# Kernel optimization log

Measured on AMD Instinct MI355X. Metric: run time of the kernel, lower is better.

Reference implementation:

```python
import jax, jax.numpy as jnp
import numpy as np

B, S, D, NL, H, KV, F, V, R = 4, 1024, 2048, 2, 16, 4, 8192, 32000, 16
HD = D // H                      # 128, Llama-3 head dim
LORA_SCALE = 32.0 / 16.0         # alpha / r
ROPE_THETA = 500000.0
EPS = 1e-5


def _rope_tables(seq_len, hd):
    inv = 1.0 / (ROPE_THETA ** (jnp.arange(0, hd, 2, dtype=jnp.float32) / hd))
    freqs = jnp.arange(seq_len, dtype=jnp.float32)[:, None] * inv[None, :]   # [S, hd/2]
    emb = jnp.concatenate([freqs, freqs], axis=-1)                           # [S, hd]
    return jnp.cos(emb), jnp.sin(emb)


def _apply_rope(x, cos, sin):
    # x: [B, S, nh, HD]; LLaMA rotate_half convention
    h = x.shape[-1] // 2
    rot = jnp.concatenate([-x[..., h:], x[..., :h]], axis=-1)
    return x * cos[None, :, None, :] + rot * sin[None, :, None, :]


def _rmsnorm(x, w):
    return x * jax.lax.rsqrt(jnp.mean(x * x, axis=-1, keepdims=True) + EPS) * w


def _forward(embed, wq, wk, wv, wo, laq, lbq, lav, lbv, wg, wu, wd, n1, n2, nf,
             input_ids, attention_mask):
    b, s = input_ids.shape
    cos, sin = _rope_tables(s, HD)
    amask = attention_mask.astype(bool)
    # causal AND key-padding mask: [B, 1, S, S]
    mask = jnp.tril(jnp.ones((s, s), bool))[None, None] & amask[:, None, None, :]
    x = embed[input_ids]                                   # [B, S, D]
    for l in range(NL):
        h = _rmsnorm(x, n1[l])
        # base projection + LoRA adapter (q and v only, as in target_modules)
        q = h @ wq[l] + ((h @ laq[l].T) @ lbq[l].T) * LORA_SCALE
        k = h @ wk[l]
        v = h @ wv[l] + ((h @ lav[l].T) @ lbv[l].T) * LORA_SCALE
        q = _apply_rope(q.reshape(b, s, H, HD), cos, sin)
        k = _apply_rope(k.reshape(b, s, KV, HD), cos, sin)
        v = v.reshape(b, s, KV, HD)
        k = jnp.repeat(k, H // KV, axis=2)                 # GQA expand
        v = jnp.repeat(v, H // KV, axis=2)
        scores = jnp.einsum('bqhd,bkhd->bhqk', q, k) / jnp.float32(np.sqrt(HD))
        scores = jnp.where(mask, scores, jnp.float32(-1e9))
        attn = jax.nn.softmax(scores, axis=-1)
        o = jnp.einsum('bhqk,bkhd->bqhd', attn, v).reshape(b, s, D)
        x = x + o @ wo[l]
        h2 = _rmsnorm(x, n2[l])
        x = x + (jax.nn.silu(h2 @ wg[l]) * (h2 @ wu[l])) @ wd[l]
    h = _rmsnorm(x, nf)                                    # final norm -> last_hidden_state
    m = attention_mask.astype(jnp.float32)[..., None]
    return (h * m).sum(axis=1) / jnp.clip(m.sum(axis=1), 1e-9)   # masked mean pool [B, D]


def setup_inputs() -> dict:
    key = jax.random.key(0)
    ks = jax.random.split(key, 14)
    sd = 0.02
    nrm = lambda k, shape: sd * jax.random.normal(k, shape, dtype=jnp.float32)
    return {
        'embed': nrm(ks[0], (V, D)),
        'wq': nrm(ks[1], (NL, D, D)),
        'wk': nrm(ks[2], (NL, D, KV * HD)),
        'wv': nrm(ks[3], (NL, D, KV * HD)),
        'wo': nrm(ks[4], (NL, D, D)),
        'laq': nrm(ks[5], (NL, R, D)),
        'lbq': nrm(ks[6], (NL, D, R)),
        'lav': nrm(ks[7], (NL, R, D)),
        'lbv': nrm(ks[8], (NL, KV * HD, R)),
        'wg': nrm(ks[9], (NL, D, F)),
        'wu': nrm(ks[10], (NL, D, F)),
        'wd': nrm(ks[11], (NL, F, D)),
        'n1': jnp.ones((NL, D), jnp.float32),
        'n2': jnp.ones((NL, D), jnp.float32),
        'nf': jnp.ones((D,), jnp.float32),
        'input_ids': jax.random.randint(ks[12], (B, S), 0, V, dtype=jnp.int32),
        'attention_mask': jnp.ones((B, S), jnp.int32),
    }


def reference(embed, wq, wk, wv, wo, laq, lbq, lav, lbv, wg, wu, wd, n1, n2, nf,
              input_ids, attention_mask):
    return _forward(embed, wq, wk, wv, wo, laq, lbq, lav, lbv, wg, wu, wd,
                    n1, n2, nf, input_ids, attention_mask)
```

## Files before the change

kernel.cpp:

```cpp
#include <hip/hip_runtime.h>
#include <math.h>

#define B_  4
#define S_  1024
#define D_  2048
#define NL_ 2
#define H_  16
#define KV_ 4
#define F_  8192
#define R_  16
#define HD_ 128
#define BS_ (B_*S_)
#define QT2 32
#define KBLK 64
#define NQKV 3072

typedef unsigned short u16;
typedef __attribute__((ext_vector_type(8))) __bf16 bf16x8;
typedef __attribute__((ext_vector_type(4))) float  f32x4;

__device__ __forceinline__ u16 f2bf(float f) {
    unsigned x = __float_as_uint(f);
    unsigned r = (x + 0x7fffu + ((x >> 16) & 1u)) >> 16;
    return (u16)r;
}
__device__ __forceinline__ float bf2f(u16 u) {
    return __uint_as_float(((unsigned)u) << 16);
}

__device__ __forceinline__ void gload16(const void* g, void* l) {
    __builtin_amdgcn_global_load_lds((const __attribute__((address_space(1))) void*)g,
                                     (__attribute__((address_space(3))) void*)l, 16, 0, 0);
}

__global__ void embed_kernel(const float* __restrict__ embed,
                             const int* __restrict__ ids,
                             float* __restrict__ x) {
    int tok = blockIdx.x;
    int id  = ids[tok];
    const float4* src = (const float4*)(embed + (size_t)id * D_);
    float4*       dst = (float4*)(x + (size_t)tok * D_);
    for (int i = threadIdx.x; i < D_/4; i += blockDim.x) dst[i] = src[i];
}

template<int OUTBF>
__global__ __launch_bounds__(256) void rmsnorm_kernel(const float* __restrict__ x,
                                                      const float* __restrict__ w,
                                                      void* __restrict__ out) {
    int row = blockIdx.x;
    const float4* xr = (const float4*)(x + (size_t)row * D_);
    float ss = 0.f;
    for (int i = threadIdx.x; i < D_/4; i += 256) {
        float4 v = xr[i];
        ss += v.x*v.x + v.y*v.y + v.z*v.z + v.w*v.w;
    }
    __shared__ float red[4];
    for (int off = 32; off; off >>= 1) ss += __shfl_down(ss, off);
    if ((threadIdx.x & 63) == 0) red[threadIdx.x >> 6] = ss;
    __syncthreads();
    float tot = red[0] + red[1] + red[2] + red[3];
    float scale = rsqrtf(tot / (float)D_ + 1e-5f);
    const float4* w4 = (const float4*)w;
    for (int i = threadIdx.x; i < D_/4; i += 256) {
        float4 v = xr[i], g = w4[i];
        float a = v.x*scale*g.x, b = v.y*scale*g.y, c = v.z*scale*g.z, d = v.w*scale*g.w;
        if (OUTBF) {
            ushort4 o; o.x = f2bf(a); o.y = f2bf(b); o.z = f2bf(c); o.w = f2bf(d);
            ((ushort4*)((u16*)out + (size_t)row * D_))[i] = o;
        } else {
            float4 o; o.x = a; o.y = b; o.z = c; o.w = d;
            ((float4*)((float*)out + (size_t)row * D_))[i] = o;
        }
    }
}

__global__ __launch_bounds__(256) void convt_kernel(const float* __restrict__ in,
                                                    u16* __restrict__ outT,
                                                    int K, int N) {
    __shared__ float tile[64][65];
    int k0 = blockIdx.y * 64, n0 = blockIdx.x * 64;
    int t = threadIdx.x, r = t >> 4, c4 = (t & 15) * 4;
    #pragma unroll
    for (int p = 0; p < 4; p++) {
        float4 v = *(const float4*)(in + (size_t)(k0 + p * 16 + r) * N + n0 + c4);
        tile[p*16+r][c4]   = v.x; tile[p*16+r][c4+1] = v.y;
        tile[p*16+r][c4+2] = v.z; tile[p*16+r][c4+3] = v.w;
    }
    __syncthreads();
    #pragma unroll
    for (int p = 0; p < 4; p++) {
        int n = p * 16 + r;
        ushort4 o;
        o.x = f2bf(tile[c4][n]);   o.y = f2bf(tile[c4+1][n]);
        o.z = f2bf(tile[c4+2][n]); o.w = f2bf(tile[c4+3][n]);
        *(ushort4*)(outT + (size_t)(n0 + n) * K + k0 + c4) = o;
    }
}

__global__ __launch_bounds__(256) void convt_qkv(const float* __restrict__ wq,
                                                 const float* __restrict__ wk,
                                                 const float* __restrict__ wv,
                                                 const float* __restrict__ wo,
                                                 u16* __restrict__ outT) {
    int z = blockIdx.z;
    int N = (z == 0 || z == 3) ? 2048 : 512;
    if (blockIdx.x * 64 >= N) return;
    const float* in = (z == 0) ? wq : (z == 1 ? wk : (z == 2 ? wv : wo));
    size_t roff = (z == 0) ? 0 : (z == 1 ? 2048 : (z == 2 ? 2560 : 3072));
    u16* out = outT + roff * D_;
    __shared__ float tile[64][65];
    int k0 = blockIdx.y * 64, n0 = blockIdx.x * 64;
    int t = threadIdx.x, r = t >> 4, c4 = (t & 15) * 4;
    #pragma unroll
    for (int p = 0; p < 4; p++) {
        float4 v = *(const float4*)(in + (size_t)(k0 + p * 16 + r) * N + n0 + c4);
        tile[p*16+r][c4]   = v.x; tile[p*16+r][c4+1] = v.y;
        tile[p*16+r][c4+2] = v.z; tile[p*16+r][c4+3] = v.w;
    }
    __syncthreads();
    #pragma unroll
    for (int p = 0; p < 4; p++) {
        int n = p * 16 + r;
        ushort4 o;
        o.x = f2bf(tile[c4][n]);   o.y = f2bf(tile[c4+1][n]);
        o.z = f2bf(tile[c4+2][n]); o.w = f2bf(tile[c4+3][n]);
        *(ushort4*)(out + (size_t)(n0 + n) * D_ + k0 + c4) = o;
    }
}

__global__ __launch_bounds__(256) void convt_gu2(const float* __restrict__ G,
                                                 const float* __restrict__ U,
                                                 u16* __restrict__ outT) {
    __shared__ float tile[64][65];
    int k0 = blockIdx.y * 64, n0 = blockIdx.x * 64;
    int t = threadIdx.x, r = t >> 4, c4 = (t & 15) * 4;
    #pragma unroll
    for (int slot = 0; slot < 2; slot++) {
        const float* in = slot ? U : G;
        if (slot) __syncthreads();
        #pragma unroll
        for (int p = 0; p < 4; p++) {
            float4 v = *(const float4*)(in + (size_t)(k0 + p * 16 + r) * F_ + n0 + c4);
            tile[p*16+r][c4]   = v.x; tile[p*16+r][c4+1] = v.y;
            tile[p*16+r][c4+2] = v.z; tile[p*16+r][c4+3] = v.w;
        }
        __syncthreads();
        #pragma unroll
        for (int p = 0; p < 4; p++) {
            int n = p * 16 + r;
            int orow = n0 + n;
            int wrow = ((orow >> 7) << 8) + slot * 128 + (orow & 127);
            ushort4 o;
            o.x = f2bf(tile[c4][n]);   o.y = f2bf(tile[c4+1][n]);
            o.z = f2bf(tile[c4+2][n]); o.w = f2bf(tile[c4+3][n]);
            *(ushort4*)(outT + (size_t)wrow * D_ + k0 + c4) = o;
        }
    }
}

template<int ACC>
__global__ __launch_bounds__(256) void gemm_bt(const u16* __restrict__ A,
                                               const u16* __restrict__ Bt,
                                               float* __restrict__ C,
                                               int N, int K) {
    __shared__ __align__(16) u16 As[128*64];
    __shared__ __align__(16) u16 Bs[128*64];
    int tid = threadIdx.x, lane = tid & 63;
    int wid = tid >> 6, wm = wid >> 1, wn = wid & 1;
    int m0 = blockIdx.y * 128, n0 = blockIdx.x * 128;
    const u16* Ab = A  + (size_t)m0 * K;
    const u16* Bb = Bt + (size_t)n0 * K;
    f32x4 acc[4][4] = {};
    for (int k0 = 0; k0 < K; k0 += 64) {
        #pragma unroll
        for (int qq = 0; qq < 4; qq++) {
            int u = qq * 256 + tid;
            int row = u >> 3, cu = u & 7, scu = cu ^ (row & 7);
            size_t goff = (size_t)row * K + k0 + scu * 8;
            gload16(Ab + goff, (char*)As + u * 16);
            gload16(Bb + goff, (char*)Bs + u * 16);
        }
        __syncthreads();
        #pragma unroll
        for (int kk = 0; kk < 2; kk++) {
            int cu = kk * 4 + (lane >> 4);
            bf16x8 af[4], bfr[4];
            #pragma unroll
            for (int i = 0; i < 4; i++) {
                int ar = wm * 64 + i * 16 + (lane & 15);
                af[i]  = *(const bf16x8*)((const char*)As + (((ar << 3) | (cu ^ (ar & 7))) << 4));
                int br = wn * 64 + i * 16 + (lane & 15);
                bfr[i] = *(const bf16x8*)((const char*)Bs + (((br << 3) | (cu ^ (br & 7))) << 4));
            }
            #pragma unroll
            for (int i = 0; i < 4; i++)
                #pragma unroll
                for (int j = 0; j < 4; j++)
                    acc[i][j] = __builtin_amdgcn_mfma_f32_16x16x32_bf16(af[i], bfr[j], acc[i][j], 0, 0, 0);
        }
        __syncthreads();
    }
    int r0 = (lane >> 4) * 4, c0 = lane & 15;
    #pragma unroll
    for (int i = 0; i < 4; i++)
        #pragma unroll
        for (int j = 0; j < 4; j++) {
            int row = m0 + wm * 64 + i * 16 + r0;
            int col = n0 + wn * 64 + j * 16 + c0;
            float* cp = C + (size_t)row * N + col;
            #pragma unroll
            for (int r = 0; r < 4; r++) {
                if (ACC) cp[(size_t)r * N] += acc[i][j][r];
                else     cp[(size_t)r * N] = acc[i][j][r];
            }
        }
}

__global__ __launch_bounds__(512) void gemm_gateup8(const u16* __restrict__ A,
                                                    const u16* __restrict__ Wt,
                                                    u16* __restrict__ act,
                                                    int Nact, int K) {
    __shared__ __align__(16) u16 ring[2][4][8192];
    int tid = threadIdx.x, lane = tid & 63;
    int w = tid >> 6;
    int wm = w >> 2, wn = w & 3;
    int g = lane >> 4, li = lane & 15;
    int m0 = blockIdx.y * 256, n0 = blockIdx.x * 256;
    const u16* Ab = A  + (size_t)m0 * K;
    const u16* Bb = Wt + (size_t)n0 * K;
    int nt = K >> 6;

    f32x4 acc[8][4] = {};

    #define STG(s, t_, kh, P)                                                        \
        do {                                                                         \
            int u_ = (P) * 512 + tid;                                                \
            int j_ = u_ >> 3, cc_ = u_ & 7;                                          \
            int sc_ = cc_ ^ (j_ & 7);                                                \
            int row_ = 2 * j_ + (sc_ >> 2);                                          \
            int kc_ = (t_) * 64 + (kh) * 32 + (sc_ & 3) * 8;                         \
            gload16(Ab + (size_t)row_ * K + kc_, (char*)&ring[0][s][0] + u_ * 16);   \
            gload16(Bb + (size_t)row_ * K + kc_, (char*)&ring[1][s][0] + u_ * 16);   \
        } while (0)

    #define FRAG(op, s, r) (*(const bf16x8*)((const char*)&ring[op][s][0] +          \
        (((((r) >> 1) << 3) | (((((r) & 1) << 2) | g) ^ (((r) >> 1) & 7))) << 4)))

    STG(0, 0, 0, 0); STG(0, 0, 0, 1);
    STG(1, 0, 1, 0); STG(1, 0, 1, 1);
    STG(2, 1, 0, 0); STG(2, 1, 0, 1);

    for (int t = 0; t < nt; t++) {
        int s0  = (2 * t) & 3;
        int s1  = (2 * t + 1) & 3;
        int sW0 = (2 * t + 3) & 3;
        int sW1 = s0;
        bf16x8 af[4], bfr[4];

        if (t == nt - 1) asm volatile("s_waitcnt vmcnt(4)" ::: "memory");
        else             asm volatile("s_waitcnt vmcnt(8)" ::: "memory");
        __builtin_amdgcn_s_barrier();
        __builtin_amdgcn_sched_barrier(0);
        #pragma unroll
        for (int j = 0; j < 4; j++) bfr[j] = FRAG(1, s0, wn * 64 + j * 16 + li);
        #pragma unroll
        for (int i = 0; i < 4; i++) af[i] = FRAG(0, s0, wm * 128 + i * 16 + li);
        if (t + 1 < nt) STG(sW0, t + 1, 1, 0);
        asm volatile("s_waitcnt lgkmcnt(0)" ::: "memory");
        __builtin_amdgcn_sched_barrier(0);
        __builtin_amdgcn_s_setprio(1);
        #pragma unroll
        for (int i = 0; i < 4; i++)
            #pragma unroll
            for (int j = 0; j < 4; j++)
                acc[i][j] = __builtin_amdgcn_mfma_f32_16x16x32_bf16(af[i], bfr[j], acc[i][j], 0, 0, 0);
        __builtin_amdgcn_s_setprio(0);

        __builtin_amdgcn_s_barrier();
        __builtin_amdgcn_sched_barrier(0);
        #pragma unroll
        for (int i = 0; i < 4; i++) af[i] = FRAG(0, s0, wm * 128 + 64 + i * 16 + li);
        if (t + 1 < nt) STG(sW0, t + 1, 1, 1);
        asm volatile("s_waitcnt lgkmcnt(0)" ::: "memory");
        __builtin_amdgcn_sched_barrier(0);
        __builtin_amdgcn_s_setprio(1);
        #pragma unroll
        for (int i = 0; i < 4; i++)
            #pragma unroll
            for (int j = 0; j < 4; j++)
                acc[4 + i][j] = __builtin_amdgcn_mfma_f32_16x16x32_bf16(af[i], bfr[j], acc[4 + i][j], 0, 0, 0);
        __builtin_amdgcn_s_setprio(0);

        if (t == nt - 1) asm volatile("s_waitcnt vmcnt(0)" ::: "memory");
        else             asm volatile("s_waitcnt vmcnt(8)" ::: "memory");
        __builtin_amdgcn_s_barrier();
        __builtin_amdgcn_sched_barrier(0);
        #pragma unroll
        for (int j = 0; j < 4; j++) bfr[j] = FRAG(1, s1, wn * 64 + j * 16 + li);
        #pragma unroll
        for (int i = 0; i < 4; i++) af[i] = FRAG(0, s1, wm * 128 + i * 16 + li);
        if (t + 2 < nt) STG(sW1, t + 2, 0, 0);
        asm volatile("s_waitcnt lgkmcnt(0)" ::: "memory");
        __builtin_amdgcn_sched_barrier(0);
        __builtin_amdgcn_s_setprio(1);
        #pragma unroll
        for (int i = 0; i < 4; i++)
            #pragma unroll
            for (int j = 0; j < 4; j++)
                acc[i][j] = __builtin_amdgcn_mfma_f32_16x16x32_bf16(af[i], bfr[j], acc[i][j], 0, 0, 0);
        __builtin_amdgcn_s_setprio(0);

        __builtin_amdgcn_s_barrier();
        __builtin_amdgcn_sched_barrier(0);
        #pragma unroll
        for (int i = 0; i < 4; i++) af[i] = FRAG(0, s1, wm * 128 + 64 + i * 16 + li);
        if (t + 2 < nt) STG(sW1, t + 2, 0, 1);
        asm volatile("s_waitcnt lgkmcnt(0)" ::: "memory");
        __builtin_amdgcn_sched_barrier(0);
        __builtin_amdgcn_s_setprio(1);
        #pragma unroll
        for (int i = 0; i < 4; i++)
            #pragma unroll
            for (int j = 0; j < 4; j++)
                acc[4 + i][j] = __builtin_amdgcn_mfma_f32_16x16x32_bf16(af[i], bfr[j], acc[4 + i][j], 0, 0, 0);
        __builtin_amdgcn_s_setprio(0);
    }
    #undef STG
    #undef FRAG

    __syncthreads();
    float* X = (float*)&ring[0][0][0];
    if (wn >= 2) {
        float* Rr = X + (size_t)(wm * 2 + (wn - 2)) * 8192;
        #pragma unroll
        for (int i = 0; i < 8; i++)
            #pragma unroll
            for (int j = 0; j < 4; j++)
                #pragma unroll
                for (int r = 0; r < 4; r++) {
                    int row = i * 16 + g * 4 + r;
                    int col = j * 16 + li;
                    Rr[row * 64 + (col ^ (((row >> 2) & 3) << 4))] = acc[i][j][r];
                }
    }
    __syncthreads();
    if (wn < 2) {
        const float* Rr = X + (size_t)(wm * 2 + wn) * 8192;
        int colbase = (n0 >> 1) + wn * 64;
        #pragma unroll
        for (int i = 0; i < 8; i++)
            #pragma unroll
            for (int j = 0; j < 4; j++)
                #pragma unroll
                for (int r = 0; r < 4; r++) {
                    int row = i * 16 + g * 4 + r;
                    int col = j * 16 + li;
                    float gv = acc[i][j][r];
                    float uv = Rr[row * 64 + (col ^ (((row >> 2) & 3) << 4))];
                    float s = gv / (1.f + __expf(-gv));
                    act[(size_t)(m0 + wm * 128 + row) * Nact + colbase + col] = f2bf(s * uv);
                }
    }
}

__global__ __launch_bounds__(512) void gemm_down_ring(const u16* __restrict__ A,
                                                      const u16* __restrict__ Bt,
                                                      float* __restrict__ C,
                                                      int N, int K) {
    __shared__ __align__(16) u16 ringA[4][8192];
    __shared__ __align__(16) u16 ringB[4][4096];
    int tid = threadIdx.x, lane = tid & 63;
    int w = tid >> 6;
    int wm = w >> 1, wn = w & 1;
    int g = lane >> 4, li = lane & 15;
    int m0 = blockIdx.y * 256, n0 = blockIdx.x * 128;
    const u16* Ab = A  + (size_t)m0 * K;
    const u16* Bb = Bt + (size_t)n0 * K;
    int nt = K >> 6;

    f32x4 acc[4][4] = {};

    #define STGA(s, t_, kh, P)                                                       \
        do {                                                                         \
            int u_ = (P) * 512 + tid;                                                \
            int j_ = u_ >> 3, cc_ = u_ & 7;                                          \
            int sc_ = cc_ ^ (j_ & 7);                                                \
            int row_ = 2 * j_ + (sc_ >> 2);                                          \
            int kc_ = (t_) * 64 + (kh) * 32 + (sc_ & 3) * 8;                         \
            gload16(Ab + (size_t)row_ * K + kc_, (char*)&ringA[s][0] + u_ * 16);     \
        } while (0)
    #define STGB(s, t_, kh)                                                          \
        do {                                                                         \
            int u_ = tid;                                                            \
            int j_ = u_ >> 3, cc_ = u_ & 7;                                          \
            int sc_ = cc_ ^ (j_ & 7);                                                \
            int row_ = 2 * j_ + (sc_ >> 2);                                          \
            int kc_ = (t_) * 64 + (kh) * 32 + (sc_ & 3) * 8;                         \
            gload16(Bb + (size_t)row_ * K + kc_, (char*)&ringB[s][0] + u_ * 16);     \
        } while (0)

    #define FRAGA(s, r) (*(const bf16x8*)((const char*)&ringA[s][0] +                \
        (((((r) >> 1) << 3) | (((((r) & 1) << 2) | g) ^ (((r) >> 1) & 7))) << 4)))
    #define FRAGB(s, r) (*(const bf16x8*)((const char*)&ringB[s][0] +                \
        (((((r) >> 1) << 3) | (((((r) & 1) << 2) | g) ^ (((r) >> 1) & 7))) << 4)))

    STGA(0, 0, 0, 0); STGA(0, 0, 0, 1); STGB(0, 0, 0);
    STGA(1, 0, 1, 0); STGA(1, 0, 1, 1); STGB(1, 0, 1);
    STGA(2, 1, 0, 0); STGA(2, 1, 0, 1); STGB(2, 1, 0);

    for (int t = 0; t < nt; t++) {
        int s0  = (2 * t) & 3;
        int s1  = (2 * t + 1) & 3;
        int sW0 = (2 * t + 3) & 3;
        int sW1 = s0;
        bf16x8 af[4], bfr[4];

        if (t == nt - 1) asm volatile("s_waitcnt vmcnt(3)" ::: "memory");
        else             asm volatile("s_waitcnt vmcnt(6)" ::: "memory");
        __builtin_amdgcn_s_barrier();
        __builtin_amdgcn_sched_barrier(0);
        #pragma unroll
        for (int j = 0; j < 4; j++) bfr[j] = FRAGB(s0, wn * 64 + j * 16 + li);
        #pragma unroll
        for (int i = 0; i < 4; i++) af[i] = FRAGA(s0, wm * 64 + i * 16 + li);
        if (t + 1 < nt) { STGA(sW0, t + 1, 1, 0); STGA(sW0, t + 1, 1, 1); STGB(sW0, t + 1, 1); }
        asm volatile("s_waitcnt lgkmcnt(0)" ::: "memory");
        __builtin_amdgcn_sched_barrier(0);
        __builtin_amdgcn_s_setprio(1);
        #pragma unroll
        for (int i = 0; i < 4; i++)
            #pragma unroll
            for (int j = 0; j < 4; j++)
                acc[i][j] = __builtin_amdgcn_mfma_f32_16x16x32_bf16(af[i], bfr[j], acc[i][j], 0, 0, 0);
        __builtin_amdgcn_s_setprio(0);

        if (t == nt - 1) asm volatile("s_waitcnt vmcnt(0)" ::: "memory");
        else             asm volatile("s_waitcnt vmcnt(6)" ::: "memory");
        __builtin_amdgcn_s_barrier();
        __builtin_amdgcn_sched_barrier(0);
        #pragma unroll
        for (int j = 0; j < 4; j++) bfr[j] = FRAGB(s1, wn * 64 + j * 16 + li);
        #pragma unroll
        for (int i = 0; i < 4; i++) af[i] = FRAGA(s1, wm * 64 + i * 16 + li);
        if (t + 2 < nt) { STGA(sW1, t + 2, 0, 0); STGA(sW1, t + 2, 0, 1); STGB(sW1, t + 2, 0); }
        asm volatile("s_waitcnt lgkmcnt(0)" ::: "memory");
        __builtin_amdgcn_sched_barrier(0);
        __builtin_amdgcn_s_setprio(1);
        #pragma unroll
        for (int i = 0; i < 4; i++)
            #pragma unroll
            for (int j = 0; j < 4; j++)
                acc[i][j] = __builtin_amdgcn_mfma_f32_16x16x32_bf16(af[i], bfr[j], acc[i][j], 0, 0, 0);
        __builtin_amdgcn_s_setprio(0);
    }
    #undef STGA
    #undef STGB
    #undef FRAGA
    #undef FRAGB

    int r0 = g * 4, c0 = li;
    #pragma unroll
    for (int i = 0; i < 4; i++)
        #pragma unroll
        for (int j = 0; j < 4; j++) {
            int row = m0 + wm * 64 + i * 16 + r0;
            int col = n0 + wn * 64 + j * 16 + c0;
            float* cp = C + (size_t)row * N + col;
            #pragma unroll
            for (int r = 0; r < 4; r++)
                cp[(size_t)r * N] += acc[i][j][r];
        }
}

__global__ __launch_bounds__(256) void lora_a2(const u16* __restrict__ h,
                                               const float* __restrict__ laq,
                                               const float* __restrict__ lav,
                                               float* __restrict__ t16q,
                                               float* __restrict__ t16v) {
    const float* la = blockIdx.y ? lav : laq;
    float* t16 = blockIdx.y ? t16v : t16q;
    int r = threadIdx.x >> 4;
    int c = threadIdx.x & 15;
    int row = blockIdx.x * 16 + r;
    const ushort4* hr = (const ushort4*)(h + (size_t)row * D_);
    const float4* lr = (const float4*)(la + (size_t)c * D_);
    float acc = 0.f;
    #pragma unroll 4
    for (int i = 0; i < D_/4; i++) {
        ushort4 a = hr[i]; float4 b = lr[i];
        acc += bf2f(a.x)*b.x + bf2f(a.y)*b.y + bf2f(a.z)*b.z + bf2f(a.w)*b.w;
    }
    t16[(size_t)row * R_ + c] = acc;
}

__global__ void qkconv_rope(const float* __restrict__ qkv,
                            const float* __restrict__ t16q,
                            const float* __restrict__ lbq,
                            u16* __restrict__ Qc, u16* __restrict__ Kc) {
    int tok = blockIdx.x, hh = blockIdx.y, t = threadIdx.x;
    int b = tok >> 10, s = tok & (S_ - 1);
    __shared__ float ts[R_];
    if (t < R_) ts[t] = t16q[(size_t)tok * R_ + t];
    __syncthreads();
    float inv = __expf(-(float)t * (13.122363377404328f / 64.0f));
    float f = (float)s * inv;
    float c = __cosf(f), si = __sinf(f);
    float x0, x1;
    u16* dst;
    if (hh < H_) {
        const float* src = qkv + (size_t)tok * NQKV + hh * HD_;
        int d0 = hh * HD_ + t;
        float l0 = 0.f, l1 = 0.f;
        const float4* b0 = (const float4*)(lbq + (size_t)d0 * R_);
        const float4* b1 = (const float4*)(lbq + (size_t)(d0 + 64) * R_);
        #pragma unroll
        for (int r4 = 0; r4 < 4; r4++) {
            float4 v0 = b0[r4], v1 = b1[r4];
            l0 += v0.x*ts[r4*4] + v0.y*ts[r4*4+1] + v0.z*ts[r4*4+2] + v0.w*ts[r4*4+3];
            l1 += v1.x*ts[r4*4] + v1.y*ts[r4*4+1] + v1.z*ts[r4*4+2] + v1.w*ts[r4*4+3];
        }
        x0 = src[t] + 2.0f * l0;
        x1 = src[t + 64] + 2.0f * l1;
        dst = Qc + (((size_t)(b * H_ + hh)) * S_ + s) * HD_;
    } else {
        int kh = hh - H_;
        const float* src = qkv + (size_t)tok * NQKV + 2048 + kh * HD_;
        x0 = src[t];
        x1 = src[t + 64];
        dst = Kc + (((size_t)(b * KV_ + kh)) * S_ + s) * HD_;
    }
    dst[t]      = f2bf(x0 * c - x1 * si);
    dst[t + 64] = f2bf(x1 * c + x0 * si);
}

__global__ __launch_bounds__(256) void vconv_t(const float* __restrict__ qkv,
                                               const float* __restrict__ t16v,
                                               const float* __restrict__ lbv,
                                               u16* __restrict__ Vt) {
    __shared__ float tile[32][33];
    __shared__ float ts[32][16];
    int s0 = blockIdx.x * 32, d0 = blockIdx.y * 32;
    int bk = blockIdx.z;
    int b = bk >> 2, kvh = bk & 3;
    int t = threadIdx.x;
    #pragma unroll
    for (int p = 0; p < 2; p++) {
        int idx = p * 256 + t;
        ts[idx >> 4][idx & 15] = t16v[(size_t)(b * S_ + s0 + (idx >> 4)) * R_ + (idx & 15)];
    }
    int r = t >> 3, c4 = (t & 7) * 4;
    float4 v = *(const float4*)(qkv + (size_t)(b * S_ + s0 + r) * NQKV + 2560 + kvh * HD_ + d0 + c4);
    __syncthreads();
    float vv[4] = {v.x, v.y, v.z, v.w};
    #pragma unroll
    for (int e = 0; e < 4; e++) {
        int d = kvh * HD_ + d0 + c4 + e;
        const float4* lr = (const float4*)(lbv + (size_t)d * R_);
        float l = 0.f;
        #pragma unroll
        for (int r4 = 0; r4 < 4; r4++) {
            float4 w = lr[r4];
            l += w.x*ts[r][r4*4] + w.y*ts[r][r4*4+1] + w.z*ts[r][r4*4+2] + w.w*ts[r][r4*4+3];
        }
        vv[e] += 2.0f * l;
    }
    tile[r][c4] = vv[0]; tile[r][c4+1] = vv[1]; tile[r][c4+2] = vv[2]; tile[r][c4+3] = vv[3];
    __syncthreads();
    int dr = t >> 3, s4 = (t & 7) * 4;
    ushort4 o;
    o.x = f2bf(tile[s4][dr]);   o.y = f2bf(tile[s4+1][dr]);
    o.z = f2bf(tile[s4+2][dr]); o.w = f2bf(tile[s4+3][dr]);
    *(ushort4*)(Vt + (((size_t)(b * KV_ + kvh)) * HD_ + d0 + dr) * S_ + s0 + s4) = o;
}

__global__ __launch_bounds__(512) void flash_attn(const u16* __restrict__ Qc,
                                                  const u16* __restrict__ Kc,
                                                  const u16* __restrict__ Vt,
                                                  const int* __restrict__ am,
                                                  u16* __restrict__ o) {
    __shared__ __align__(16) u16 Ks[64 * 128];
    __shared__ __align__(16) u16 Vs[128 * 64];
    __shared__ __align__(16) u16 Ps[8][16][72];
    __shared__ int am_s[KBLK];
    int qt = gridDim.x - 1 - blockIdx.x;
    int kvh = blockIdx.y, b = blockIdx.z;
    int tid = threadIdx.x, lane = tid & 63, w = tid >> 6;
    int g = lane >> 4, li = lane & 15;
    int h = kvh * 4 + (w & 3);
    int qrow0 = qt * QT2 + (w >> 2) * 16;

    bf16x8 qf[4];
    const u16* qb = Qc + (((size_t)(b * H_ + h)) * S_ + qrow0 + li) * HD_;
    #pragma unroll
    for (int dd = 0; dd < 4; dd++) qf[dd] = *(const bf16x8*)(qb + dd * 32 + g * 8);

    float m_r[4], l_r[4];
    f32x4 oacc[8];
    #pragma unroll
    for (int r = 0; r < 4; r++) { m_r[r] = -1e30f; l_r[r] = 0.f; }
    #pragma unroll
    for (int d = 0; d < 8; d++) oacc[d] = (f32x4){0.f, 0.f, 0.f, 0.f};

    const u16* Kg = Kc + ((size_t)(b * KV_ + kvh)) * S_ * HD_;
    const u16* Vg = Vt + ((size_t)(b * KV_ + kvh)) * HD_ * S_;
    int qg0 = qrow0 + g * 4;
    int nkv = (qt * QT2 + QT2 - 1) >> 6;

    for (int kvt = 0; kvt <= nkv; kvt++) {
        int kv0 = kvt * KBLK;
        #pragma unroll
        for (int qq = 0; qq < 2; qq++) {
            int u = qq * 512 + tid;
            int krow = u >> 4, p = u & 15;
            gload16(Kg + (size_t)(kv0 + krow) * HD_ + (p ^ (krow & 7)) * 8, (char*)Ks + u * 16);
            int vrow = u >> 3, pv = u & 7;
            gload16(Vg + (size_t)vrow * S_ + kv0 + (pv ^ (vrow & 7)) * 8, (char*)Vs + u * 16);
        }
        if (tid < KBLK) am_s[tid] = am[b * S_ + kv0 + tid];
        __syncthreads();

        if (kv0 <= qrow0 + 15) {
            float ps[4][4];
            #pragma unroll
            for (int kt = 0; kt < 4; kt++) {
                f32x4 sa = (f32x4){0.f, 0.f, 0.f, 0.f};
                int row = kt * 16 + li;
                #pragma unroll
                for (int dd = 0; dd < 4; dd++) {
                    int c = dd * 4 + g;
                    bf16x8 kf = *(const bf16x8*)((const char*)Ks + ((row * 16 + (c ^ (row & 7))) << 4));
                    sa = __builtin_amdgcn_mfma_f32_16x16x32_bf16(qf[dd], kf, sa, 0, 0, 0);
                }
                int kcol = kv0 + kt * 16 + li;
                int amok = am_s[kt * 16 + li];
                #pragma unroll
                for (int r = 0; r < 4; r++) {
                    float s = sa[r] * 0.08838834764831845f;
                    ps[kt][r] = (amok && kcol <= qg0 + r) ? s : -1e9f;
                }
            }

            float rmax[4], rsum[4], scl[4];
            #pragma unroll
            for (int r = 0; r < 4; r++)
                rmax[r] = fmaxf(fmaxf(ps[0][r], ps[1][r]), fmaxf(ps[2][r], ps[3][r]));
            #pragma unroll
            for (int msk = 1; msk < 16; msk <<= 1)
                #pragma unroll
                for (int r = 0; r < 4; r++) rmax[r] = fmaxf(rmax[r], __shfl_xor(rmax[r], msk));
            #pragma unroll
            for (int r = 0; r < 4; r++) {
                float mn = fmaxf(m_r[r], rmax[r]);
                scl[r] = __expf(m_r[r] - mn);
                m_r[r] = mn;
                rsum[r] = 0.f;
            }
            #pragma unroll
            for (int kt = 0; kt < 4; kt++)
                #pragma unroll
                for (int r = 0; r < 4; r++) {
                    float p = __expf(ps[kt][r] - m_r[r]);
                    ps[kt][r] = p;
                    rsum[r] += p;
                }
            #pragma unroll
            for (int msk = 1; msk < 16; msk <<= 1)
                #pragma unroll
                for (int r = 0; r < 4; r++) rsum[r] += __shfl_xor(rsum[r], msk);
            #pragma unroll
            for (int r = 0; r < 4; r++) l_r[r] = l_r[r] * scl[r] + rsum[r];
            #pragma unroll
            for (int d = 0; d < 8; d++)
                #pragma unroll
                for (int r = 0; r < 4; r++) oacc[d][r] *= scl[r];

            #pragma unroll
            for (int kt = 0; kt < 4; kt++)
                #pragma unroll
                for (int r = 0; r < 4; r++)
                    Ps[w][g * 4 + r][kt * 16 + li] = f2bf(ps[kt][r]);
            bf16x8 pf[2];
            #pragma unroll
            for (int ks = 0; ks < 2; ks++)
                pf[ks] = *(const bf16x8*)&Ps[w][li][ks * 32 + g * 8];

            #pragma unroll
            for (int dblk = 0; dblk < 8; dblk++) {
                int row = dblk * 16 + li;
                #pragma unroll
                for (int ks = 0; ks < 2; ks++) {
                    int c = ks * 4 + g;
                    bf16x8 vf = *(const bf16x8*)((const char*)Vs + ((row * 8 + (c ^ (row & 7))) << 4));
                    oacc[dblk] = __builtin_amdgcn_mfma_f32_16x16x32_bf16(pf[ks], vf, oacc[dblk], 0, 0, 0);
                }
            }
        }
        __syncthreads();
    }

    float invl[4];
    #pragma unroll
    for (int r = 0; r < 4; r++) invl[r] = 1.f / l_r[r];
    #pragma unroll
    for (int dblk = 0; dblk < 8; dblk++)
        #pragma unroll
        for (int r = 0; r < 4; r++) {
            int qrow = qg0 + r;
            o[(((size_t)b * S_ + qrow) * H_ + h) * HD_ + dblk * 16 + li] =
                f2bf(oacc[dblk][r] * invl[r]);
        }
}

__global__ __launch_bounds__(256) void pool_kernel(const float* __restrict__ h,
                                                   const int* __restrict__ am,
                                                   float* __restrict__ out) {
    int b = blockIdx.y;
    int d = blockIdx.x * 256 + threadIdx.x;
    float acc = 0.f, ms = 0.f;
    for (int s = 0; s < S_; s++) {
        float mm = (float)am[b * S_ + s];
        ms  += mm;
        acc += mm * h[((size_t)b * S_ + s) * D_ + d];
    }
    out[(size_t)b * D_ + d] = acc / fmaxf(ms, 1e-9f);
}

extern "C" void kernel_launch(void* const* d_in, const int* in_sizes, int n_in,
                              void* d_out, int out_size, void* d_ws, size_t ws_size,
                              hipStream_t stream) {
    const float* embed = (const float*)d_in[0];
    const float* wq    = (const float*)d_in[1];
    const float* wk    = (const float*)d_in[2];
    const float* wv    = (const float*)d_in[3];
    const float* wo    = (const float*)d_in[4];
    const float* laq   = (const float*)d_in[5];
    const float* lbq   = (const float*)d_in[6];
    const float* lav   = (const float*)d_in[7];
    const float* lbv   = (const float*)d_in[8];
    const float* wg    = (const float*)d_in[9];
    const float* wu    = (const float*)d_in[10];
    const float* wd    = (const float*)d_in[11];
    const float* n1    = (const float*)d_in[12];
    const float* n2    = (const float*)d_in[13];
    const float* nf    = (const float*)d_in[14];
    const int*   ids   = (const int*)d_in[15];
    const int*   am    = (const int*)d_in[16];
    float* out = (float*)d_out;

    char* base = (char*)d_ws;
    float* x    = (float*)base;
    u16*   hbf  = (u16*)(base + 33554432);
    u16*   obf  = (u16*)(base + 50331648);
    char*  Rg   = base + 67108864;
    float* qkv  = (float*)Rg;
    float* t16v = (float*)(base + 117440512);
    u16*   act  = (u16*)Rg;
    float* hf   = (float*)Rg;
    float* t16q = (float*)(base + 134217728);
    u16*   wT0  = (u16*)(base + 134479872);
    u16*   Qc   = (u16*)(base + 201588736);
    u16*   Kc   = (u16*)(base + 218365952);
    u16*   Vtb  = (u16*)(base + 222560256);

    embed_kernel<<<BS_, 256, 0, stream>>>(embed, ids, x);

    for (int l = 0; l < NL_; l++) {
        const float* wql = wq + (size_t)l * D_ * D_;
        const float* wkl = wk + (size_t)l * D_ * (KV_*HD_);
        const float* wvl = wv + (size_t)l * D_ * (KV_*HD_);
        const float* wol = wo + (size_t)l * D_ * D_;
        const float* wgl = wg + (size_t)l * D_ * F_;
        const float* wul = wu + (size_t)l * D_ * F_;
        const float* wdl = wd + (size_t)l * F_ * D_;

        rmsnorm_kernel<1><<<BS_, 256, 0, stream>>>(x, n1 + (size_t)l * D_, hbf);

        convt_qkv<<<dim3(32, 32, 4), 256, 0, stream>>>(wql, wkl, wvl, wol, wT0);
        gemm_bt<0><<<dim3(NQKV/128, BS_/128), 256, 0, stream>>>(hbf, wT0, qkv, NQKV, D_);

        lora_a2<<<dim3(BS_/16, 2), 256, 0, stream>>>(hbf, laq + (size_t)l * R_ * D_,
                                                     lav + (size_t)l * R_ * D_, t16q, t16v);

        qkconv_rope<<<dim3(BS_, H_ + KV_), 64, 0, stream>>>(qkv, t16q,
                                                            lbq + (size_t)l * D_ * R_, Qc, Kc);
        vconv_t<<<dim3(S_/32, HD_/32, B_*KV_), 256, 0, stream>>>(qkv, t16v,
                                                                 lbv + (size_t)l * (KV_*HD_) * R_, Vtb);

        flash_attn<<<dim3(S_/QT2, KV_, B_), 512, 0, stream>>>(Qc, Kc, Vtb, am, obf);

        gemm_bt<1><<<dim3(D_/128, BS_/128), 256, 0, stream>>>(obf, wT0 + (size_t)3072 * D_, x, D_, D_);

        rmsnorm_kernel<1><<<BS_, 256, 0, stream>>>(x, n2 + (size_t)l * D_, hbf);
        convt_gu2<<<dim3(F_/64, D_/64), 256, 0, stream>>>(wgl, wul, wT0);
        gemm_gateup8<<<dim3((2*F_)/256, BS_/256), 512, 0, stream>>>(hbf, wT0, act, F_, D_);
        convt_kernel<<<dim3(D_/64, F_/64), 256, 0, stream>>>(wdl, wT0, F_, D_);
        gemm_down_ring<<<dim3(D_/128, BS_/256), 512, 0, stream>>>(act, wT0, x, D_, F_);
    }

    rmsnorm_kernel<0><<<BS_, 256, 0, stream>>>(x, nf, hf);
    pool_kernel<<<dim3(D_/256, B_), 256, 0, stream>>>(hf, am, out);
}
```

Before: 1.902 ms.

## Emit bf16 QKV, prefetch gate-up A fragments early, reuse ring GEMM for o-proj

The QKV projection GEMM now writes bf16 instead of fp32, and the RoPE and V-transpose kernels read bf16, roughly halving that intermediate's write and read traffic. The gate/up GEMM loads the second half of its A fragments into a separate register set before the barrier, so LDS reads overlap more with the MFMA phase at the cost of extra registers. The output projection now reuses the pipelined gemm_down_ring kernel, which accumulates into x, in place of the simple gemm_bt. Rounding Q/K/V to bf16 before the LoRA add and RoPE adds some precision loss.

```diff
diff --git a/kernel.cpp b/kernel.cpp
--- a/kernel.cpp
+++ b/kernel.cpp
@@ -158,11 +158,10 @@
     }
 }
 
-template<int ACC>
-__global__ __launch_bounds__(256) void gemm_bt(const u16* __restrict__ A,
-                                               const u16* __restrict__ Bt,
-                                               float* __restrict__ C,
-                                               int N, int K) {
+__global__ __launch_bounds__(256) void gemm_bt_bf16(const u16* __restrict__ A,
+                                                    const u16* __restrict__ Bt,
+                                                    u16* __restrict__ C,
+                                                    int N, int K) {
     __shared__ __align__(16) u16 As[128*64];
     __shared__ __align__(16) u16 Bs[128*64];
     int tid = threadIdx.x, lane = tid & 63;
@@ -207,12 +206,10 @@
         for (int j = 0; j < 4; j++) {
             int row = m0 + wm * 64 + i * 16 + r0;
             int col = n0 + wn * 64 + j * 16 + c0;
-            float* cp = C + (size_t)row * N + col;
-            #pragma unroll
-            for (int r = 0; r < 4; r++) {
-                if (ACC) cp[(size_t)r * N] += acc[i][j][r];
-                else     cp[(size_t)r * N] = acc[i][j][r];
-            }
+            u16* cp = C + (size_t)row * N + col;
+            #pragma unroll
+            for (int r = 0; r < 4; r++)
+                cp[(size_t)r * N] = f2bf(acc[i][j][r]);
         }
 }
 
@@ -255,7 +252,7 @@
         int s1  = (2 * t + 1) & 3;
         int sW0 = (2 * t + 3) & 3;
         int sW1 = s0;
-        bf16x8 af[4], bfr[4];
+        bf16x8 afA[4], afB[4], bfr[4];
 
         if (t == nt - 1) asm volatile("s_waitcnt vmcnt(4)" ::: "memory");
         else             asm volatile("s_waitcnt vmcnt(8)" ::: "memory");
@@ -264,7 +261,7 @@
         #pragma unroll
         for (int j = 0; j < 4; j++) bfr[j] = FRAG(1, s0, wn * 64 + j * 16 + li);
         #pragma unroll
-        for (int i = 0; i < 4; i++) af[i] = FRAG(0, s0, wm * 128 + i * 16 + li);
+        for (int i = 0; i < 4; i++) afA[i] = FRAG(0, s0, wm * 128 + i * 16 + li);
         if (t + 1 < nt) STG(sW0, t + 1, 1, 0);
         asm volatile("s_waitcnt lgkmcnt(0)" ::: "memory");
         __builtin_amdgcn_sched_barrier(0);
@@ -273,13 +270,14 @@
         for (int i = 0; i < 4; i++)
             #pragma unroll
             for (int j = 0; j < 4; j++)
-                acc[i][j] = __builtin_amdgcn_mfma_f32_16x16x32_bf16(af[i], bfr[j], acc[i][j], 0, 0, 0);
+                acc[i][j] = __builtin_amdgcn_mfma_f32_16x16x32_bf16(afA[i], bfr[j], acc[i][j], 0, 0, 0);
         __builtin_amdgcn_s_setprio(0);
+        #pragma unroll
+        for (int i = 0; i < 4; i++) afB[i] = FRAG(0, s0, wm * 128 + 64 + i * 16 + li);
+        __builtin_amdgcn_sched_barrier(0);
 
         __builtin_amdgcn_s_barrier();
         __builtin_amdgcn_sched_barrier(0);
-        #pragma unroll
-        for (int i = 0; i < 4; i++) af[i] = FRAG(0, s0, wm * 128 + 64 + i * 16 + li);
         if (t + 1 < nt) STG(sW0, t + 1, 1, 1);
         asm volatile("s_waitcnt lgkmcnt(0)" ::: "memory");
         __builtin_amdgcn_sched_barrier(0);
@@ -288,7 +286,7 @@
         for (int i = 0; i < 4; i++)
             #pragma unroll
             for (int j = 0; j < 4; j++)
-                acc[4 + i][j] = __builtin_amdgcn_mfma_f32_16x16x32_bf16(af[i], bfr[j], acc[4 + i][j], 0, 0, 0);
+                acc[4 + i][j] = __builtin_amdgcn_mfma_f32_16x16x32_bf16(afB[i], bfr[j], acc[4 + i][j], 0, 0, 0);
         __builtin_amdgcn_s_setprio(0);
 
         if (t == nt - 1) asm volatile("s_waitcnt vmcnt(0)" ::: "memory");
@@ -298,7 +296,7 @@
         #pragma unroll
         for (int j = 0; j < 4; j++) bfr[j] = FRAG(1, s1, wn * 64 + j * 16 + li);
         #pragma unroll
-        for (int i = 0; i < 4; i++) af[i] = FRAG(0, s1, wm * 128 + i * 16 + li);
+        for (int i = 0; i < 4; i++) afA[i] = FRAG(0, s1, wm * 128 + i * 16 + li);
         if (t + 2 < nt) STG(sW1, t + 2, 0, 0);
         asm volatile("s_waitcnt lgkmcnt(0)" ::: "memory");
         __builtin_amdgcn_sched_barrier(0);
@@ -307,13 +305,14 @@
         for (int i = 0; i < 4; i++)
             #pragma unroll
             for (int j = 0; j < 4; j++)
-                acc[i][j] = __builtin_amdgcn_mfma_f32_16x16x32_bf16(af[i], bfr[j], acc[i][j], 0, 0, 0);
+                acc[i][j] = __builtin_amdgcn_mfma_f32_16x16x32_bf16(afA[i], bfr[j], acc[i][j], 0, 0, 0);
         __builtin_amdgcn_s_setprio(0);
+        #pragma unroll
+        for (int i = 0; i < 4; i++) afB[i] = FRAG(0, s1, wm * 128 + 64 + i * 16 + li);
+        __builtin_amdgcn_sched_barrier(0);
 
         __builtin_amdgcn_s_barrier();
         __builtin_amdgcn_sched_barrier(0);
-        #pragma unroll
-        for (int i = 0; i < 4; i++) af[i] = FRAG(0, s1, wm * 128 + 64 + i * 16 + li);
         if (t + 2 < nt) STG(sW1, t + 2, 0, 1);
         asm volatile("s_waitcnt lgkmcnt(0)" ::: "memory");
         __builtin_amdgcn_sched_barrier(0);
@@ -322,7 +321,7 @@
         for (int i = 0; i < 4; i++)
             #pragma unroll
             for (int j = 0; j < 4; j++)
-                acc[4 + i][j] = __builtin_amdgcn_mfma_f32_16x16x32_bf16(af[i], bfr[j], acc[4 + i][j], 0, 0, 0);
+                acc[4 + i][j] = __builtin_amdgcn_mfma_f32_16x16x32_bf16(afB[i], bfr[j], acc[4 + i][j], 0, 0, 0);
         __builtin_amdgcn_s_setprio(0);
     }
     #undef STG
@@ -493,7 +492,7 @@
     t16[(size_t)row * R_ + c] = acc;
 }
 
-__global__ void qkconv_rope(const float* __restrict__ qkv,
+__global__ void qkconv_rope(const u16* __restrict__ qkvb,
                             const float* __restrict__ t16q,
                             const float* __restrict__ lbq,
                             u16* __restrict__ Qc, u16* __restrict__ Kc) {
@@ -508,7 +507,7 @@
     float x0, x1;
     u16* dst;
     if (hh < H_) {
-        const float* src = qkv + (size_t)tok * NQKV + hh * HD_;
+        const u16* src = qkvb + (size_t)tok * NQKV + hh * HD_;
         int d0 = hh * HD_ + t;
         float l0 = 0.f, l1 = 0.f;
         const float4* b0 = (const float4*)(lbq + (size_t)d0 * R_);
@@ -519,21 +518,21 @@
             l0 += v0.x*ts[r4*4] + v0.y*ts[r4*4+1] + v0.z*ts[r4*4+2] + v0.w*ts[r4*4+3];
             l1 += v1.x*ts[r4*4] + v1.y*ts[r4*4+1] + v1.z*ts[r4*4+2] + v1.w*ts[r4*4+3];
         }
-        x0 = src[t] + 2.0f * l0;
-        x1 = src[t + 64] + 2.0f * l1;
+        x0 = bf2f(src[t]) + 2.0f * l0;
+        x1 = bf2f(src[t + 64]) + 2.0f * l1;
         dst = Qc + (((size_t)(b * H_ + hh)) * S_ + s) * HD_;
     } else {
         int kh = hh - H_;
-        const float* src = qkv + (size_t)tok * NQKV + 2048 + kh * HD_;
-        x0 = src[t];
-        x1 = src[t + 64];
+        const u16* src = qkvb + (size_t)tok * NQKV + 2048 + kh * HD_;
+        x0 = bf2f(src[t]);
+        x1 = bf2f(src[t + 64]);
         dst = Kc + (((size_t)(b * KV_ + kh)) * S_ + s) * HD_;
     }
     dst[t]      = f2bf(x0 * c - x1 * si);
     dst[t + 64] = f2bf(x1 * c + x0 * si);
 }
 
-__global__ __launch_bounds__(256) void vconv_t(const float* __restrict__ qkv,
+__global__ __launch_bounds__(256) void vconv_t(const u16* __restrict__ qkvb,
                                                const float* __restrict__ t16v,
                                                const float* __restrict__ lbv,
                                                u16* __restrict__ Vt) {
@@ -549,9 +548,9 @@
         ts[idx >> 4][idx & 15] = t16v[(size_t)(b * S_ + s0 + (idx >> 4)) * R_ + (idx & 15)];
     }
     int r = t >> 3, c4 = (t & 7) * 4;
-    float4 v = *(const float4*)(qkv + (size_t)(b * S_ + s0 + r) * NQKV + 2560 + kvh * HD_ + d0 + c4);
+    ushort4 v4 = *(const ushort4*)(qkvb + (size_t)(b * S_ + s0 + r) * NQKV + 2560 + kvh * HD_ + d0 + c4);
     __syncthreads();
-    float vv[4] = {v.x, v.y, v.z, v.w};
+    float vv[4] = {bf2f(v4.x), bf2f(v4.y), bf2f(v4.z), bf2f(v4.w)};
     #pragma unroll
     for (int e = 0; e < 4; e++) {
         int d = kvh * HD_ + d0 + c4 + e;
@@ -752,7 +751,7 @@
     u16*   hbf  = (u16*)(base + 33554432);
     u16*   obf  = (u16*)(base + 50331648);
     char*  Rg   = base + 67108864;
-    float* qkv  = (float*)Rg;
+    u16*   qkvb = (u16*)Rg;
     float* t16v = (float*)(base + 117440512);
     u16*   act  = (u16*)Rg;
     float* hf   = (float*)Rg;
@@ -776,19 +775,19 @@
         rmsnorm_kernel<1><<<BS_, 256, 0, stream>>>(x, n1 + (size_t)l * D_, hbf);
 
         convt_qkv<<<dim3(32, 32, 4), 256, 0, stream>>>(wql, wkl, wvl, wol, wT0);
-        gemm_bt<0><<<dim3(NQKV/128, BS_/128), 256, 0, stream>>>(hbf, wT0, qkv, NQKV, D_);
+        gemm_bt_bf16<<<dim3(NQKV/128, BS_/128), 256, 0, stream>>>(hbf, wT0, qkvb, NQKV, D_);
 
         lora_a2<<<dim3(BS_/16, 2), 256, 0, stream>>>(hbf, laq + (size_t)l * R_ * D_,
                                                      lav + (size_t)l * R_ * D_, t16q, t16v);
 
-        qkconv_rope<<<dim3(BS_, H_ + KV_), 64, 0, stream>>>(qkv, t16q,
+        qkconv_rope<<<dim3(BS_, H_ + KV_), 64, 0, stream>>>(qkvb, t16q,
                                                             lbq + (size_t)l * D_ * R_, Qc, Kc);
-        vconv_t<<<dim3(S_/32, HD_/32, B_*KV_), 256, 0, stream>>>(qkv, t16v,
+        vconv_t<<<dim3(S_/32, HD_/32, B_*KV_), 256, 0, stream>>>(qkvb, t16v,
                                                                  lbv + (size_t)l * (KV_*HD_) * R_, Vtb);
 
         flash_attn<<<dim3(S_/QT2, KV_, B_), 512, 0, stream>>>(Qc, Kc, Vtb, am, obf);
 
-        gemm_bt<1><<<dim3(D_/128, BS_/128), 256, 0, stream>>>(obf, wT0 + (size_t)3072 * D_, x, D_, D_);
+        gemm_down_ring<<<dim3(D_/128, BS_/256), 512, 0, stream>>>(obf, wT0 + (size_t)3072 * D_, x, D_, D_);
 
         rmsnorm_kernel<1><<<BS_, 256, 0, stream>>>(x, n2 + (size_t)l * D_, hbf);
         convt_gu2<<<dim3(F_/64, D_/64), 256, 0, stream>>>(wgl, wul, wT0);
```

Result: no change. 1.873 ms (-1.5%).
